# Performance work log

Measured on AMD Instinct MI355X. Metric: run time of the kernel, lower is better.

The kernel has to match this reference:

```python
import jax, jax.numpy as jnp
import numpy as np

HEADS = 8
HEIGHT = 512
WIDTH = 512
LATENT = 64  # height // 8
N_INST = 8


def setup_inputs() -> dict:
    key = jax.random.key(0)
    ks = jax.random.split(key, 8)
    C, Cx, L, N = 320, 768, 77, N_INST
    HW = LATENT * LATENT
    hidden_states = jax.random.normal(ks[0], (2, HW, C), jnp.float32)
    encoder_hidden_states = jax.random.normal(ks[1], (N + 3, L, Cx), jnp.float32)
    # non-degenerate normalized boxes (x0, y0, x1, y1)
    rng = np.random.default_rng(0)
    x0 = rng.uniform(0.0, 0.5, (N,)).astype(np.float32)
    y0 = rng.uniform(0.0, 0.5, (N,)).astype(np.float32)
    x1 = (x0 + rng.uniform(0.2, 0.45, (N,))).astype(np.float32)
    y1 = (y0 + rng.uniform(0.2, 0.45, (N,))).astype(np.float32)
    bboxes = jnp.asarray(np.stack([x0, y0, x1, y1], axis=-1)[None], jnp.float32)  # (1, N, 4)
    s = 0.02
    Wq = jax.random.normal(ks[2], (C, C), jnp.float32) * s
    Wk = jax.random.normal(ks[3], (Cx, C), jnp.float32) * s
    Wv = jax.random.normal(ks[4], (Cx, C), jnp.float32) * s
    Wo = jax.random.normal(ks[5], (C, C), jnp.float32) * s
    bo = jnp.zeros((C,), jnp.float32)
    return dict(hidden_states=hidden_states, encoder_hidden_states=encoder_hidden_states,
                bboxes=bboxes, Wq=Wq, Wk=Wk, Wv=Wv, Wo=Wo, bo=bo)


def _heads(x):
    # (B, S, H*D) -> (B*H, S, D)   [diffusers head_to_batch_dim]
    B, S, C = x.shape
    D = C // HEADS
    return x.reshape(B, S, HEADS, D).transpose(0, 2, 1, 3).reshape(B * HEADS, S, D)


def _unheads(x):
    # (B*H, S, D) -> (B, S, H*D)   [diffusers batch_to_head_dim]
    BH, S, D = x.shape
    B = BH // HEADS
    return x.reshape(B, HEADS, S, D).transpose(0, 2, 1, 3).reshape(B, S, HEADS * D)


def _forward(hidden_states, encoder_hidden_states, bboxes, Wq, Wk, Wv, Wo, bo):
    N = bboxes.shape[1]
    HW = hidden_states.shape[1]
    # drop the extra (MIGC) text embedding row, as in the processor
    ehs = encoder_hidden_states[:-1]  # (N+2, L, Cx)
    # batch = [uncond, cond repeated instance_num+1 times]
    hs = jnp.concatenate([hidden_states[:1],
                          jnp.repeat(hidden_states[1:2], N + 1, axis=0)], axis=0)  # (N+2, HW, C)
    q = _heads(hs @ Wq)
    k = _heads(ehs @ Wk)
    v = _heads(ehs @ Wv)
    scale = 1.0 / jnp.sqrt(jnp.asarray(q.shape[-1], q.dtype))
    probs = jax.nn.softmax(jnp.einsum('bqd,bkd->bqk', q, k) * scale, axis=-1)  # ((N+2)*H, HW, L)
    out = _unheads(jnp.einsum('bqk,bkd->bqd', probs, v))  # (N+2, HW, C)
    out = out @ Wo + bo
    hs_uncond = out[:1]
    cond_ca = out[1:][None]  # (1, N+1, HW, C)
    # rasterize per-instance bbox masks at full res (int() truncation == floor for positives)
    b = bboxes[0]  # (N, 4) = x0, y0, x1, y1
    w_min = jnp.floor(WIDTH * b[:, 0])[:, None, None]
    w_max = jnp.floor(WIDTH * b[:, 2])[:, None, None]
    h_min = jnp.floor(HEIGHT * b[:, 1])[:, None, None]
    h_max = jnp.floor(HEIGHT * b[:, 3])[:, None, None]
    rows = jnp.arange(HEIGHT, dtype=jnp.float32)[None, :, None]
    cols = jnp.arange(WIDTH, dtype=jnp.float32)[None, None, :]
    masks = ((rows >= h_min) & (rows < h_max) & (cols >= w_min) & (cols < w_max)).astype(jnp.float32)  # (N,H,W)
    gmask = jax.image.resize(masks, (N, LATENT, LATENT), method='bilinear')  # (N, 64, 64)
    # NaiveFuser: phase weights = [0.1 (full prompt), 10*mask_i], normalized sum over phases
    phase_w = jnp.concatenate([jnp.full((1, HW), 0.1, jnp.float32),
                               gmask.reshape(N, HW) * 10.0], axis=0)  # (N+1, HW)
    w = phase_w[None, :, :, None]  # (1, N+1, HW, 1)
    fused = (cond_ca * w).sum(axis=1) / (w.sum(axis=1) + 1e-6)  # (1, HW, C)
    return jnp.concatenate([hs_uncond, fused], axis=0)  # (2, HW, C)


def reference(hidden_states, encoder_hidden_states, bboxes, Wq, Wk, Wv, Wo, bo):
    return _forward(hidden_states, encoder_hidden_states, bboxes, Wq, Wk, Wv, Wo, bo)
```

## Files before the change

kernel.cpp:

```cpp
#include <hip/hip_runtime.h>
#include <math.h>

#define HW 4096
#define C 320
#define CX 768
#define L 77
#define NB 10
#define NH 8
#define HD 40
#define NINST 8
#define SCALE 0.15811388300841898f
#define PSTR 104
#define KSTR 48
#define VSTR 104
#define XSTR 328
#define KBH (80 * KSTR)
#define VBH (48 * VSTR)
#define KVCP 264

#define SEG_KV   130
#define MASK_U0  130
#define PAD_U0   146
#define WPK_U0   226
#define NPREP    276

typedef _Float16 half8v __attribute__((ext_vector_type(8)));
typedef _Float16 half4v __attribute__((ext_vector_type(4)));
typedef float f32x4 __attribute__((ext_vector_type(4)));

__device__ __forceinline__ float axis_profile(int o, float lo, float hi) {
    float num = 0.f, den = 0.f;
    int j0 = 8 * o - 4;
#pragma unroll
    for (int t = 0; t < 16; ++t) {
        int j = j0 + t;
        float wt = 1.0f - fabsf((float)t - 7.5f) * 0.125f;
        if (j >= 0 && j < 512) {
            den += wt;
            float fj = (float)j;
            if (fj >= lo && fj < hi) num += wt;
        }
    }
    return num / den;
}

__device__ __forceinline__ half8v cvt8(float4 a, float4 b) {
    half8v h = {(_Float16)a.x, (_Float16)a.y, (_Float16)a.z, (_Float16)a.w,
                (_Float16)b.x, (_Float16)b.y, (_Float16)b.z, (_Float16)b.w};
    return h;
}

__global__ __launch_bounds__(256) void prep_kernel(
        const float* __restrict__ bboxes, const float* __restrict__ ehs,
        const float* __restrict__ Wq, const float* __restrict__ Wk,
        const float* __restrict__ Wv, const float* __restrict__ Wo,
        float* __restrict__ wPh, float* __restrict__ wSum,
        _Float16* __restrict__ WqT, _Float16* __restrict__ WoT,
        _Float16* __restrict__ VTg, _Float16* __restrict__ Khp) {
    __shared__ __align__(16) unsigned char psm[34048];
    int bx = blockIdx.x, tid = threadIdx.x;

    if (bx < SEG_KV) {
        const int K = CX, M = NB * L;
        int lane = tid & 63, wave = tid >> 6;
        int m0 = (bx / 10) * 64 + wave * 16;
        int n0 = (bx % 10) * 64;
        int lr = lane & 15, kq = (lane >> 4) * 8;
        int arow = m0 + lr; if (arow >= M) arow = M - 1;
        const float* ap = ehs + (size_t)arow * K + kq;
        const float* W = (n0 < C) ? Wk : Wv;
        int colbase = (n0 < C) ? n0 : n0 - C;
        _Float16* Bs = (_Float16*)psm;
        f32x4 acc0 = {0.f,0.f,0.f,0.f}, acc1 = acc0, acc2 = acc0, acc3 = acc0;
        for (int c3 = 0; c3 < 3; ++c3) {
            int k0c = c3 * 256;
            __syncthreads();
            for (int i = tid; i < 64 * 256; i += 256) {
                int col = i & 63, k = i >> 6;
                Bs[col * KVCP + k] = (_Float16)W[(size_t)(k0c + k) * C + colbase + col];
            }
            __syncthreads();
#pragma unroll
            for (int k0 = 0; k0 < 256; k0 += 32) {
                float4 a0 = *(const float4*)(ap + k0c + k0);
                float4 a1 = *(const float4*)(ap + k0c + k0 + 4);
                half8v af = cvt8(a0, a1);
                half8v b0 = *(const half8v*)&Bs[(0 * 16 + lr) * KVCP + kq + k0];
                half8v b1 = *(const half8v*)&Bs[(1 * 16 + lr) * KVCP + kq + k0];
                half8v b2 = *(const half8v*)&Bs[(2 * 16 + lr) * KVCP + kq + k0];
                half8v b3 = *(const half8v*)&Bs[(3 * 16 + lr) * KVCP + kq + k0];
                acc0 = __builtin_amdgcn_mfma_f32_16x16x32_f16(af, b0, acc0, 0, 0, 0);
                acc1 = __builtin_amdgcn_mfma_f32_16x16x32_f16(af, b1, acc1, 0, 0, 0);
                acc2 = __builtin_amdgcn_mfma_f32_16x16x32_f16(af, b2, acc2, 0, 0, 0);
                acc3 = __builtin_amdgcn_mfma_f32_16x16x32_f16(af, b3, acc3, 0, 0, 0);
            }
        }
        int rb = m0 + ((lane >> 4) << 2);
        f32x4 accs[4] = {acc0, acc1, acc2, acc3};
#pragma unroll
        for (int t = 0; t < 4; ++t) {
            int col = n0 + t * 16 + lr;
#pragma unroll
            for (int r = 0; r < 4; ++r) {
                int row = rb + r;
                if (row < M) {
                    int bb = row / 77;
                    int key = row - bb * 77;
                    if (col < C) {
                        int h = col / HD, d = col - h * HD;
                        Khp[((size_t)(bb * 8 + h) * 80 + key) * KSTR + d] = (_Float16)accs[t][r];
                    } else {
                        int ch = col - C;
                        int h = ch / HD, d = ch - h * HD;
                        VTg[((size_t)(bb * 8 + h) * 48 + d) * VSTR + key] = (_Float16)accs[t][r];
                    }
                }
            }
        }
    } else if (bx < PAD_U0) {
        float* sw_s = (float*)psm;
        float* sh_s = (float*)psm + 512;
        int oyb = (bx - MASK_U0) * 4;
        for (int i = tid; i < NINST * 64; i += 256) {
            int n = i >> 6, ox = i & 63;
            float lo = floorf(512.f * bboxes[n * 4 + 0]);
            float hi = floorf(512.f * bboxes[n * 4 + 2]);
            sw_s[n * 64 + ox] = axis_profile(ox, lo, hi);
        }
        if (tid < NINST * 4) {
            int n = tid >> 2, oy = tid & 3;
            float lo = floorf(512.f * bboxes[n * 4 + 1]);
            float hi = floorf(512.f * bboxes[n * 4 + 3]);
            sh_s[n * 4 + oy] = axis_profile(oyb + oy, lo, hi);
        }
        __syncthreads();
        int oy = tid >> 6, ox = tid & 63;
        int hw = (oyb + oy) * 64 + ox;
        float sum = 0.1f;
        wPh[hw] = 0.1f;
#pragma unroll
        for (int n = 0; n < NINST; ++n) {
            float wv = 10.f * sh_s[n * 4 + oy] * sw_s[n * 64 + ox];
            wPh[(n + 1) * HW + hw] = wv;
            sum += wv;
        }
        wSum[hw] = sum;
    } else if (bx < WPK_U0) {
        int bh = bx - PAD_U0;
        _Float16* Vb = VTg + (size_t)bh * VBH;
        for (int i = tid; i < 832; i += 256) {
            int dd = i / 104, key = i - dd * 104;
            Vb[(size_t)(40 + dd) * VSTR + key] = (_Float16)((dd == 0 && key < 77) ? 1.f : 0.f);
        }
        for (int i = tid; i < 1080; i += 256) {
            int dd = i / 27, key = 77 + i - dd * 27;
            Vb[(size_t)dd * VSTR + key] = (_Float16)0.f;
        }
        _Float16* Kb = Khp + (size_t)bh * KBH;
        for (int i = tid; i < 144; i += 256) {
            int key = 77 + i / 48, dd = i - (i / 48) * 48;
            Kb[(size_t)key * KSTR + dd] = (_Float16)0.f;
        }
    } else {
        float (*tile)[65] = (float (*)[65])psm;
        int zz = bx - WPK_U0;
        int z = zz / 25, inner = zz - z * 25;
        int by = inner / 5, bx2 = inner - by * 5;
        const float* W = z ? Wo : Wq;
        _Float16* WT = z ? WoT : WqT;
        int kt = by * 64, nt = bx2 * 64;
#pragma unroll
        for (int p = 0; p < 16; ++p) {
            int idx = p * 256 + tid;
            int k = idx >> 6, n = idx & 63;
            tile[k][n] = W[(size_t)(kt + k) * C + nt + n];
        }
        __syncthreads();
#pragma unroll
        for (int p = 0; p < 16; ++p) {
            int idx = p * 256 + tid;
            int n = idx >> 6, k = idx & 63;
            WT[(size_t)(nt + n) * C + kt + k] = (_Float16)tile[k][n];
        }
    }
}

__global__ __launch_bounds__(512, 1) void attn_oproj(
        const float* __restrict__ hs,
        const _Float16* __restrict__ WqT,
        const _Float16* __restrict__ Khp,
        const _Float16* __restrict__ VTg,
        const float* __restrict__ wPh,
        const float* __restrict__ wSum,
        const _Float16* __restrict__ WoT,
        const float* __restrict__ bo,
        float* __restrict__ Out) {
    __shared__ _Float16 smem[NH * 2 * 16 * PSTR + 32 * XSTR];
    _Float16* Xs = smem + NH * 2 * 16 * PSTR;

    const int tid = threadIdx.x;
    const int wave = tid >> 6, lane = tid & 63;
    const int head = wave;
    const int qrow0 = blockIdx.x * 16;
    const int c = lane & 15, quad = lane >> 4;
    _Float16* pl0 = smem + (size_t)(wave * 2) * 16 * PSTR;
    _Float16* pl1 = pl0 + 16 * PSTR;
    half8v zero8 = {(_Float16)0.f,(_Float16)0.f,(_Float16)0.f,(_Float16)0.f,
                    (_Float16)0.f,(_Float16)0.f,(_Float16)0.f,(_Float16)0.f};

#pragma unroll
    for (int i = 0; i < 4; ++i) {
        int idx = i * 64 + lane;
        if (idx < 224) {
            int buf = idx / 112;
            int rem = idx - buf * 112;
            int row = rem / 7, ch = rem - row * 7;
            _Float16* pb = buf ? pl1 : pl0;
            *(half8v*)&pb[row * PSTR + 40 + ch * 8] = zero8;
        }
    }

    {
        const float* bu = hs + (size_t)(qrow0 + c) * C + quad * 8;
        const float* bc = bu + (size_t)HW * C;
        f32x4 qa0[3] = {}, qa1[3] = {};
        for (int k0 = 0; k0 < C; k0 += 32) {
            float4 u0 = *(const float4*)(bu + k0);
            float4 u1 = *(const float4*)(bu + k0 + 4);
            float4 c0 = *(const float4*)(bc + k0);
            float4 c1 = *(const float4*)(bc + k0 + 4);
            half8v hu = cvt8(u0, u1);
            half8v hc = cvt8(c0, c1);
#pragma unroll
            for (int t = 0; t < 3; ++t) {
                const _Float16* ap = WqT + (size_t)(head * HD + t * 16 + c) * C + quad * 8 + k0;
                half8v af = *(const half8v*)ap;
                qa0[t] = __builtin_amdgcn_mfma_f32_16x16x32_f16(af, hu, qa0[t], 0, 0, 0);
                qa1[t] = __builtin_amdgcn_mfma_f32_16x16x32_f16(af, hc, qa1[t], 0, 0, 0);
            }
        }
#pragma unroll
        for (int t = 0; t < 3; ++t) {
            if (t < 2 || quad < 2) {
                half4v h0 = {(_Float16)(qa0[t][0] * SCALE), (_Float16)(qa0[t][1] * SCALE),
                             (_Float16)(qa0[t][2] * SCALE), (_Float16)(qa0[t][3] * SCALE)};
                half4v h1 = {(_Float16)(qa1[t][0] * SCALE), (_Float16)(qa1[t][1] * SCALE),
                             (_Float16)(qa1[t][2] * SCALE), (_Float16)(qa1[t][3] * SCALE)};
                *(half4v*)(pl0 + c * PSTR + t * 16 + quad * 4) = h0;
                *(half4v*)(pl1 + c * PSTR + t * 16 + quad * 4) = h1;
            }
        }
    }
    half8v qu0 = *(const half8v*)(pl0 + (size_t)c * PSTR + quad * 8);
    half8v qu1 = *(const half8v*)(pl0 + (size_t)c * PSTR + 32 + quad * 8);
    half8v qc0 = *(const half8v*)(pl1 + (size_t)c * PSTR + quad * 8);
    half8v qc1 = *(const half8v*)(pl1 + (size_t)c * PSTR + 32 + quad * 8);

    f32x4 oacc[3] = {};
    const int srcl = 32 + c;

    for (int b = 0; b < NB; ++b) {
        const _Float16* Kb = Khp + (size_t)(b * 8 + head) * KBH;
        const _Float16* Vb = VTg + (size_t)(b * 8 + head) * VBH;
        half8v qb0 = b ? qc0 : qu0;
        half8v qb1 = b ? qc1 : qu1;
        float w = b ? wPh[(size_t)(b - 1) * HW + qrow0 + c] : 1.f;

        f32x4 s[5];
#pragma unroll
        for (int u = 0; u < 5; ++u) {
            half8v ka0 = *(const half8v*)&Kb[(u * 16 + c) * KSTR + quad * 8];
            half8v ka1 = *(const half8v*)&Kb[(u * 16 + c) * KSTR + 32 + quad * 8];
            f32x4 a = {0.f,0.f,0.f,0.f};
            a = __builtin_amdgcn_mfma_f32_16x16x32_f16(ka0, qb0, a, 0, 0, 0);
            a = __builtin_amdgcn_mfma_f32_16x16x32_f16(ka1, qb1, a, 0, 0, 0);
            s[u] = a;
        }

#pragma unroll
        for (int u = 0; u < 5; ++u) {
            half4v h = {(_Float16)__expf(s[u][0]), (_Float16)__expf(s[u][1]),
                        (_Float16)__expf(s[u][2]), (_Float16)__expf(s[u][3])};
            *(half4v*)(pl0 + c * PSTR + u * 16 + quad * 4) = h;
        }
        half8v p0 = *(const half8v*)(pl0 + (size_t)c * PSTR + quad * 8);
        half8v p1 = *(const half8v*)(pl0 + (size_t)c * PSTR + 32 + quad * 8);
        half8v p2 = *(const half8v*)(pl0 + (size_t)c * PSTR + 64 + quad * 8);

        f32x4 ox[3];
#pragma unroll
        for (int t = 0; t < 3; ++t) {
            half8v va0 = *(const half8v*)&Vb[(t * 16 + c) * VSTR + quad * 8];
            half8v va1 = *(const half8v*)&Vb[(t * 16 + c) * VSTR + 32 + quad * 8];
            half8v va2 = *(const half8v*)&Vb[(t * 16 + c) * VSTR + 64 + quad * 8];
            f32x4 a = {0.f,0.f,0.f,0.f};
            a = __builtin_amdgcn_mfma_f32_16x16x32_f16(va0, p0, a, 0, 0, 0);
            a = __builtin_amdgcn_mfma_f32_16x16x32_f16(va1, p1, a, 0, 0, 0);
            a = __builtin_amdgcn_mfma_f32_16x16x32_f16(va2, p2, a, 0, 0, 0);
            ox[t] = a;
        }

        float l = __shfl(ox[2][0], srcl, 64);

        if (b == 0) {
            float rin = 1.0f / l;
#pragma unroll
            for (int t = 0; t < 3; ++t) {
                if (t < 2 || quad < 2) {
                    half4v h = {(_Float16)(ox[t][0] * rin), (_Float16)(ox[t][1] * rin),
                                (_Float16)(ox[t][2] * rin), (_Float16)(ox[t][3] * rin)};
                    *(half4v*)(Xs + (size_t)c * XSTR + head * HD + t * 16 + quad * 4) = h;
                }
            }
        } else {
            float rf = w / l;
#pragma unroll
            for (int t = 0; t < 3; ++t) {
                oacc[t][0] += ox[t][0] * rf;
                oacc[t][1] += ox[t][1] * rf;
                oacc[t][2] += ox[t][2] * rf;
                oacc[t][3] += ox[t][3] * rf;
            }
        }
    }

#pragma unroll
    for (int t = 0; t < 3; ++t) {
        if (t < 2 || quad < 2) {
            half4v h = {(_Float16)oacc[t][0], (_Float16)oacc[t][1],
                        (_Float16)oacc[t][2], (_Float16)oacc[t][3]};
            *(half4v*)(Xs + (size_t)(16 + c) * XSTR + head * HD + t * 16 + quad * 4) = h;
        }
    }
    __syncthreads();

    {
        int mt = wave & 1;
        int np = wave >> 1;
        f32x4 acc[5] = {};
#pragma unroll
        for (int k0 = 0; k0 < C; k0 += 32) {
            half8v af = *(const half8v*)&Xs[(size_t)(mt * 16 + c) * XSTR + k0 + quad * 8];
#pragma unroll
            for (int tt = 0; tt < 5; ++tt) {
                const _Float16* bp = WoT + (size_t)(np * 80 + tt * 16 + c) * C + k0 + quad * 8;
                half8v bf = *(const half8v*)bp;
                acc[tt] = __builtin_amdgcn_mfma_f32_16x16x32_f16(af, bf, acc[tt], 0, 0, 0);
            }
        }
#pragma unroll
        for (int tt = 0; tt < 5; ++tt) {
            int col = np * 80 + tt * 16 + c;
            float bv = bo[col];
#pragma unroll
            for (int r = 0; r < 4; ++r) {
                int rr = quad * 4 + r;
                float v = acc[tt][r];
                size_t row;
                if (mt == 0) {
                    v += bv;
                    row = (size_t)qrow0 + rr;
                } else {
                    float ws = wSum[qrow0 + rr];
                    v = (v + bv * ws) / (ws + 1e-6f);
                    row = (size_t)HW + qrow0 + rr;
                }
                Out[row * C + col] = v;
            }
        }
    }
}

extern "C" void kernel_launch(void* const* d_in, const int* in_sizes, int n_in,
                              void* d_out, int out_size, void* d_ws, size_t ws_size,
                              hipStream_t stream) {
    const float* hs   = (const float*)d_in[0];
    const float* ehs  = (const float*)d_in[1];
    const float* bbox = (const float*)d_in[2];
    const float* Wq   = (const float*)d_in[3];
    const float* Wk   = (const float*)d_in[4];
    const float* Wv   = (const float*)d_in[5];
    const float* Wo   = (const float*)d_in[6];
    const float* bo   = (const float*)d_in[7];
    float* out = (float*)d_out;

    float* wPh  = (float*)d_ws;
    float* wSum = wPh + (size_t)9 * HW;
    _Float16* WqT = (_Float16*)(wSum + HW);
    _Float16* WoT = WqT + (size_t)C * C;
    _Float16* Khp = WoT + (size_t)C * C;
    _Float16* VTg = Khp + (size_t)80 * KBH;

    prep_kernel<<<dim3(NPREP), 256, 0, stream>>>(bbox, ehs, Wq, Wk, Wv, Wo,
                                                 wPh, wSum, WqT, WoT, VTg, Khp);
    attn_oproj<<<dim3(HW / 16), 512, 0, stream>>>(hs, WqT, Khp, VTg, wPh, wSum,
                                                  WoT, bo, out);
}
```

Baseline: 147.8 us.

## Software-pipeline K loads across batches and drop LDS staging in KV projection

The attention loop is fully unrolled over the ten batches with double-buffered K fragments, so the next batch's K is fetched while the current batch's scores are computed, and V is loaded at the start of each batch. The P scratch buffer now alternates between two LDS regions. Separately, the KV projection GEMM no longer stages transposed weights in shared memory with barriers; each lane reads strided fp32 weights directly from global memory. This cuts LDS use and synchronisation, but the direct loads are uncoalesced scalar reads, and the unrolled loop raises register pressure.

```diff
diff --git a/kernel.cpp b/kernel.cpp
--- a/kernel.cpp
+++ b/kernel.cpp
@@ -16,7 +16,6 @@
 #define XSTR 328
 #define KBH (80 * KSTR)
 #define VBH (48 * VSTR)
-#define KVCP 264
 
 #define SEG_KV   130
 #define MASK_U0  130
@@ -57,7 +56,7 @@
         float* __restrict__ wPh, float* __restrict__ wSum,
         _Float16* __restrict__ WqT, _Float16* __restrict__ WoT,
         _Float16* __restrict__ VTg, _Float16* __restrict__ Khp) {
-    __shared__ __align__(16) unsigned char psm[34048];
+    __shared__ __align__(16) unsigned char psm[16640];
     int bx = blockIdx.x, tid = threadIdx.x;
 
     if (bx < SEG_KV) {
@@ -68,38 +67,38 @@
         int lr = lane & 15, kq = (lane >> 4) * 8;
         int arow = m0 + lr; if (arow >= M) arow = M - 1;
         const float* ap = ehs + (size_t)arow * K + kq;
-        const float* W = (n0 < C) ? Wk : Wv;
-        int colbase = (n0 < C) ? n0 : n0 - C;
-        _Float16* Bs = (_Float16*)psm;
+        const float* wp[4];
+        int cols[4];
+#pragma unroll
+        for (int t = 0; t < 4; ++t) {
+            int col = n0 + t * 16 + lr;
+            cols[t] = col;
+            wp[t] = (col < C) ? (Wk + col) : (Wv + (col - C));
+        }
         f32x4 acc0 = {0.f,0.f,0.f,0.f}, acc1 = acc0, acc2 = acc0, acc3 = acc0;
-        for (int c3 = 0; c3 < 3; ++c3) {
-            int k0c = c3 * 256;
-            __syncthreads();
-            for (int i = tid; i < 64 * 256; i += 256) {
-                int col = i & 63, k = i >> 6;
-                Bs[col * KVCP + k] = (_Float16)W[(size_t)(k0c + k) * C + colbase + col];
-            }
-            __syncthreads();
-#pragma unroll
-            for (int k0 = 0; k0 < 256; k0 += 32) {
-                float4 a0 = *(const float4*)(ap + k0c + k0);
-                float4 a1 = *(const float4*)(ap + k0c + k0 + 4);
-                half8v af = cvt8(a0, a1);
-                half8v b0 = *(const half8v*)&Bs[(0 * 16 + lr) * KVCP + kq + k0];
-                half8v b1 = *(const half8v*)&Bs[(1 * 16 + lr) * KVCP + kq + k0];
-                half8v b2 = *(const half8v*)&Bs[(2 * 16 + lr) * KVCP + kq + k0];
-                half8v b3 = *(const half8v*)&Bs[(3 * 16 + lr) * KVCP + kq + k0];
-                acc0 = __builtin_amdgcn_mfma_f32_16x16x32_f16(af, b0, acc0, 0, 0, 0);
-                acc1 = __builtin_amdgcn_mfma_f32_16x16x32_f16(af, b1, acc1, 0, 0, 0);
-                acc2 = __builtin_amdgcn_mfma_f32_16x16x32_f16(af, b2, acc2, 0, 0, 0);
-                acc3 = __builtin_amdgcn_mfma_f32_16x16x32_f16(af, b3, acc3, 0, 0, 0);
-            }
+        for (int k0 = 0; k0 < K; k0 += 32) {
+            float4 a0 = *(const float4*)(ap + k0);
+            float4 a1 = *(const float4*)(ap + k0 + 4);
+            half8v af = cvt8(a0, a1);
+            half8v bf0, bf1, bf2, bf3;
+#pragma unroll
+            for (int j = 0; j < 8; ++j) {
+                size_t kk = (size_t)(k0 + kq + j) * C;
+                bf0[j] = (_Float16)wp[0][kk];
+                bf1[j] = (_Float16)wp[1][kk];
+                bf2[j] = (_Float16)wp[2][kk];
+                bf3[j] = (_Float16)wp[3][kk];
+            }
+            acc0 = __builtin_amdgcn_mfma_f32_16x16x32_f16(af, bf0, acc0, 0, 0, 0);
+            acc1 = __builtin_amdgcn_mfma_f32_16x16x32_f16(af, bf1, acc1, 0, 0, 0);
+            acc2 = __builtin_amdgcn_mfma_f32_16x16x32_f16(af, bf2, acc2, 0, 0, 0);
+            acc3 = __builtin_amdgcn_mfma_f32_16x16x32_f16(af, bf3, acc3, 0, 0, 0);
         }
         int rb = m0 + ((lane >> 4) << 2);
         f32x4 accs[4] = {acc0, acc1, acc2, acc3};
 #pragma unroll
         for (int t = 0; t < 4; ++t) {
-            int col = n0 + t * 16 + lr;
+            int col = cols[t];
 #pragma unroll
             for (int r = 0; r < 4; ++r) {
                 int row = rb + r;
@@ -185,6 +184,79 @@
     }
 }
 
+#define LOADK(K0, K1, bidx)                                                    \
+    {                                                                          \
+        const _Float16* Kb_ = Khp + (size_t)((bidx) * 8 + head) * KBH;         \
+        _Pragma("unroll")                                                      \
+        for (int u = 0; u < 5; ++u) {                                          \
+            K0[u] = *(const half8v*)&Kb_[(u * 16 + c) * KSTR + quad * 8];      \
+            K1[u] = *(const half8v*)&Kb_[(u * 16 + c) * KSTR + 32 + quad * 8]; \
+        }                                                                      \
+    }
+
+#define BATCH(b, K0, K1, PB, PREFETCH_STMT)                                        \
+    {                                                                              \
+        const _Float16* Vb_ = VTg + (size_t)((b) * 8 + head) * VBH;                \
+        half8v va0_[3], va1_[3], va2_[3];                                          \
+        _Pragma("unroll")                                                          \
+        for (int t = 0; t < 3; ++t) {                                              \
+            va0_[t] = *(const half8v*)&Vb_[(t * 16 + c) * VSTR + quad * 8];        \
+            va1_[t] = *(const half8v*)&Vb_[(t * 16 + c) * VSTR + 32 + quad * 8];   \
+            va2_[t] = *(const half8v*)&Vb_[(t * 16 + c) * VSTR + 64 + quad * 8];   \
+        }                                                                          \
+        float w_ = (b) ? wPh[(size_t)((b) - 1) * HW + qrow0 + c] : 1.f;            \
+        half8v qb0_ = (b) ? qc0 : qu0;                                             \
+        half8v qb1_ = (b) ? qc1 : qu1;                                             \
+        f32x4 s_[5];                                                               \
+        _Pragma("unroll")                                                          \
+        for (int u = 0; u < 5; ++u) {                                              \
+            f32x4 a_ = {0.f, 0.f, 0.f, 0.f};                                       \
+            a_ = __builtin_amdgcn_mfma_f32_16x16x32_f16(K0[u], qb0_, a_, 0, 0, 0); \
+            a_ = __builtin_amdgcn_mfma_f32_16x16x32_f16(K1[u], qb1_, a_, 0, 0, 0); \
+            s_[u] = a_;                                                            \
+        }                                                                          \
+        PREFETCH_STMT;                                                             \
+        _Pragma("unroll")                                                          \
+        for (int u = 0; u < 5; ++u) {                                              \
+            half4v h_ = {(_Float16)__expf(s_[u][0]), (_Float16)__expf(s_[u][1]),   \
+                         (_Float16)__expf(s_[u][2]), (_Float16)__expf(s_[u][3])};  \
+            *(half4v*)((PB) + c * PSTR + u * 16 + quad * 4) = h_;                  \
+        }                                                                          \
+        half8v p0_ = *(const half8v*)((PB) + (size_t)c * PSTR + quad * 8);         \
+        half8v p1_ = *(const half8v*)((PB) + (size_t)c * PSTR + 32 + quad * 8);    \
+        half8v p2_ = *(const half8v*)((PB) + (size_t)c * PSTR + 64 + quad * 8);    \
+        f32x4 ox_[3];                                                              \
+        _Pragma("unroll")                                                          \
+        for (int t = 0; t < 3; ++t) {                                              \
+            f32x4 a_ = {0.f, 0.f, 0.f, 0.f};                                       \
+            a_ = __builtin_amdgcn_mfma_f32_16x16x32_f16(va0_[t], p0_, a_, 0, 0, 0);\
+            a_ = __builtin_amdgcn_mfma_f32_16x16x32_f16(va1_[t], p1_, a_, 0, 0, 0);\
+            a_ = __builtin_amdgcn_mfma_f32_16x16x32_f16(va2_[t], p2_, a_, 0, 0, 0);\
+            ox_[t] = a_;                                                           \
+        }                                                                          \
+        float l_ = __shfl(ox_[2][0], srcl, 64);                                    \
+        if ((b) == 0) {                                                            \
+            float rin_ = 1.0f / l_;                                                \
+            _Pragma("unroll")                                                      \
+            for (int t = 0; t < 3; ++t) {                                          \
+                if (t < 2 || quad < 2) {                                           \
+                    half4v h_ = {(_Float16)(ox_[t][0] * rin_), (_Float16)(ox_[t][1] * rin_),  \
+                                 (_Float16)(ox_[t][2] * rin_), (_Float16)(ox_[t][3] * rin_)}; \
+                    *(half4v*)(Xs + (size_t)c * XSTR + head * HD + t * 16 + quad * 4) = h_;   \
+                }                                                                  \
+            }                                                                      \
+        } else {                                                                   \
+            float rf_ = w_ / l_;                                                   \
+            _Pragma("unroll")                                                      \
+            for (int t = 0; t < 3; ++t) {                                          \
+                oacc[t][0] += ox_[t][0] * rf_;                                     \
+                oacc[t][1] += ox_[t][1] * rf_;                                     \
+                oacc[t][2] += ox_[t][2] * rf_;                                     \
+                oacc[t][3] += ox_[t][3] * rf_;                                     \
+            }                                                                      \
+        }                                                                          \
+    }
+
 __global__ __launch_bounds__(512, 1) void attn_oproj(
         const float* __restrict__ hs,
         const _Float16* __restrict__ WqT,
@@ -259,70 +331,18 @@
     f32x4 oacc[3] = {};
     const int srcl = 32 + c;
 
-    for (int b = 0; b < NB; ++b) {
-        const _Float16* Kb = Khp + (size_t)(b * 8 + head) * KBH;
-        const _Float16* Vb = VTg + (size_t)(b * 8 + head) * VBH;
-        half8v qb0 = b ? qc0 : qu0;
-        half8v qb1 = b ? qc1 : qu1;
-        float w = b ? wPh[(size_t)(b - 1) * HW + qrow0 + c] : 1.f;
-
-        f32x4 s[5];
-#pragma unroll
-        for (int u = 0; u < 5; ++u) {
-            half8v ka0 = *(const half8v*)&Kb[(u * 16 + c) * KSTR + quad * 8];
-            half8v ka1 = *(const half8v*)&Kb[(u * 16 + c) * KSTR + 32 + quad * 8];
-            f32x4 a = {0.f,0.f,0.f,0.f};
-            a = __builtin_amdgcn_mfma_f32_16x16x32_f16(ka0, qb0, a, 0, 0, 0);
-            a = __builtin_amdgcn_mfma_f32_16x16x32_f16(ka1, qb1, a, 0, 0, 0);
-            s[u] = a;
-        }
-
-#pragma unroll
-        for (int u = 0; u < 5; ++u) {
-            half4v h = {(_Float16)__expf(s[u][0]), (_Float16)__expf(s[u][1]),
-                        (_Float16)__expf(s[u][2]), (_Float16)__expf(s[u][3])};
-            *(half4v*)(pl0 + c * PSTR + u * 16 + quad * 4) = h;
-        }
-        half8v p0 = *(const half8v*)(pl0 + (size_t)c * PSTR + quad * 8);
-        half8v p1 = *(const half8v*)(pl0 + (size_t)c * PSTR + 32 + quad * 8);
-        half8v p2 = *(const half8v*)(pl0 + (size_t)c * PSTR + 64 + quad * 8);
-
-        f32x4 ox[3];
-#pragma unroll
-        for (int t = 0; t < 3; ++t) {
-            half8v va0 = *(const half8v*)&Vb[(t * 16 + c) * VSTR + quad * 8];
-            half8v va1 = *(const half8v*)&Vb[(t * 16 + c) * VSTR + 32 + quad * 8];
-            half8v va2 = *(const half8v*)&Vb[(t * 16 + c) * VSTR + 64 + quad * 8];
-            f32x4 a = {0.f,0.f,0.f,0.f};
-            a = __builtin_amdgcn_mfma_f32_16x16x32_f16(va0, p0, a, 0, 0, 0);
-            a = __builtin_amdgcn_mfma_f32_16x16x32_f16(va1, p1, a, 0, 0, 0);
-            a = __builtin_amdgcn_mfma_f32_16x16x32_f16(va2, p2, a, 0, 0, 0);
-            ox[t] = a;
-        }
-
-        float l = __shfl(ox[2][0], srcl, 64);
-
-        if (b == 0) {
-            float rin = 1.0f / l;
-#pragma unroll
-            for (int t = 0; t < 3; ++t) {
-                if (t < 2 || quad < 2) {
-                    half4v h = {(_Float16)(ox[t][0] * rin), (_Float16)(ox[t][1] * rin),
-                                (_Float16)(ox[t][2] * rin), (_Float16)(ox[t][3] * rin)};
-                    *(half4v*)(Xs + (size_t)c * XSTR + head * HD + t * 16 + quad * 4) = h;
-                }
-            }
-        } else {
-            float rf = w / l;
-#pragma unroll
-            for (int t = 0; t < 3; ++t) {
-                oacc[t][0] += ox[t][0] * rf;
-                oacc[t][1] += ox[t][1] * rf;
-                oacc[t][2] += ox[t][2] * rf;
-                oacc[t][3] += ox[t][3] * rf;
-            }
-        }
-    }
+    half8v kA0[5], kA1[5], kB0[5], kB1[5];
+    LOADK(kA0, kA1, 0);
+    BATCH(0, kA0, kA1, pl0, LOADK(kB0, kB1, 1));
+    BATCH(1, kB0, kB1, pl1, LOADK(kA0, kA1, 2));
+    BATCH(2, kA0, kA1, pl0, LOADK(kB0, kB1, 3));
+    BATCH(3, kB0, kB1, pl1, LOADK(kA0, kA1, 4));
+    BATCH(4, kA0, kA1, pl0, LOADK(kB0, kB1, 5));
+    BATCH(5, kB0, kB1, pl1, LOADK(kA0, kA1, 6));
+    BATCH(6, kA0, kA1, pl0, LOADK(kB0, kB1, 7));
+    BATCH(7, kB0, kB1, pl1, LOADK(kA0, kA1, 8));
+    BATCH(8, kA0, kA1, pl0, LOADK(kB0, kB1, 9));
+    BATCH(9, kB0, kB1, pl1, ((void)0));
 
 #pragma unroll
     for (int t = 0; t < 3; ++t) {
```

After: 146.4 us. Within noise of the previous version (-1.0%).

## Split attention batch loop across two wave groups with 1024-thread blocks

Applied to the files above, without the earlier changes.

Doubles the attention block to 1024 threads so two groups of eight waves each handle half of the ten batch entries (even/odd) for every head. The conditional partial sums from both groups go to separate shared-memory rows and are added in the output projection through an extra MFMA. This shortens each wave's serial loop over batches and adds more waves for latency hiding, at the cost of more shared memory, higher register pressure under launch_bounds(1024), and half the waves sitting idle during the projection. The Q staging for the second group also has to run correctly, and that part of the code is hidden.

```diff
diff --git a/kernel.cpp b/kernel.cpp
--- a/kernel.cpp
+++ b/kernel.cpp
@@ -185,7 +185,7 @@
     }
 }
 
-__global__ __launch_bounds__(512, 1) void attn_oproj(
+__global__ __launch_bounds__(1024) void attn_oproj(
         const float* __restrict__ hs,
         const _Float16* __restrict__ WqT,
         const _Float16* __restrict__ Khp,
@@ -195,12 +195,13 @@
         const _Float16* __restrict__ WoT,
         const float* __restrict__ bo,
         float* __restrict__ Out) {
-    __shared__ _Float16 smem[NH * 2 * 16 * PSTR + 32 * XSTR];
-    _Float16* Xs = smem + NH * 2 * 16 * PSTR;
+    __shared__ _Float16 smem[16 * 2 * 16 * PSTR + 48 * XSTR];
+    _Float16* Xs = smem + 16 * 2 * 16 * PSTR;
 
     const int tid = threadIdx.x;
     const int wave = tid >> 6, lane = tid & 63;
-    const int head = wave;
+    const int head = wave & 7;
+    const int hb = wave >> 3;
     const int qrow0 = blockIdx.x * 16;
     const int c = lane & 15, quad = lane >> 4;
     _Float16* pl0 = smem + (size_t)(wave * 2) * 16 * PSTR;
@@ -259,7 +260,9 @@
     f32x4 oacc[3] = {};
     const int srcl = 32 + c;
 
-    for (int b = 0; b < NB; ++b) {
+#pragma unroll
+    for (int i = 0; i < 5; ++i) {
+        int b = hb + 2 * i;
         const _Float16* Kb = Khp + (size_t)(b * 8 + head) * KBH;
         const _Float16* Vb = VTg + (size_t)(b * 8 + head) * VBH;
         half8v qb0 = b ? qc0 : qu0;
@@ -324,28 +327,39 @@
         }
     }
 
-#pragma unroll
-    for (int t = 0; t < 3; ++t) {
-        if (t < 2 || quad < 2) {
-            half4v h = {(_Float16)oacc[t][0], (_Float16)oacc[t][1],
-                        (_Float16)oacc[t][2], (_Float16)oacc[t][3]};
-            *(half4v*)(Xs + (size_t)(16 + c) * XSTR + head * HD + t * 16 + quad * 4) = h;
+    {
+        int xrow = (hb ? 32 : 16) + c;
+#pragma unroll
+        for (int t = 0; t < 3; ++t) {
+            if (t < 2 || quad < 2) {
+                half4v h = {(_Float16)oacc[t][0], (_Float16)oacc[t][1],
+                            (_Float16)oacc[t][2], (_Float16)oacc[t][3]};
+                *(half4v*)(Xs + (size_t)xrow * XSTR + head * HD + t * 16 + quad * 4) = h;
+            }
         }
     }
     __syncthreads();
 
-    {
+    if (hb == 0) {
         int mt = wave & 1;
         int np = wave >> 1;
         f32x4 acc[5] = {};
 #pragma unroll
         for (int k0 = 0; k0 < C; k0 += 32) {
-            half8v af = *(const half8v*)&Xs[(size_t)(mt * 16 + c) * XSTR + k0 + quad * 8];
+            half8v af0 = zero8, af1 = zero8;
+            if (mt == 0) {
+                af0 = *(const half8v*)&Xs[(size_t)c * XSTR + k0 + quad * 8];
+            } else {
+                af0 = *(const half8v*)&Xs[(size_t)(16 + c) * XSTR + k0 + quad * 8];
+                af1 = *(const half8v*)&Xs[(size_t)(32 + c) * XSTR + k0 + quad * 8];
+            }
 #pragma unroll
             for (int tt = 0; tt < 5; ++tt) {
                 const _Float16* bp = WoT + (size_t)(np * 80 + tt * 16 + c) * C + k0 + quad * 8;
                 half8v bf = *(const half8v*)bp;
-                acc[tt] = __builtin_amdgcn_mfma_f32_16x16x32_f16(af, bf, acc[tt], 0, 0, 0);
+                acc[tt] = __builtin_amdgcn_mfma_f32_16x16x32_f16(af0, bf, acc[tt], 0, 0, 0);
+                if (mt == 1)
+                    acc[tt] = __builtin_amdgcn_mfma_f32_16x16x32_f16(af1, bf, acc[tt], 0, 0, 0);
             }
         }
 #pragma unroll
@@ -393,6 +407,6 @@
 
     prep_kernel<<<dim3(NPREP), 256, 0, stream>>>(bbox, ehs, Wq, Wk, Wv, Wo,
                                                  wPh, wSum, WqT, WoT, VTg, Khp);
-    attn_oproj<<<dim3(HW / 16), 512, 0, stream>>>(hs, WqT, Khp, VTg, wPh, wSum,
-                                                  WoT, bo, out);
+    attn_oproj<<<dim3(HW / 16), 1024, 0, stream>>>(hs, WqT, Khp, VTg, wPh, wSum,
+                                                   WoT, bo, out);
 }
```

Result: slower. 163.2 us (+10.4%).

## Pre-convert hidden states to fp16 in prep and read K/V weights directly

Applied to the files above, without the earlier changes.

Adds a segment of prep blocks that converts both hidden-state batches to fp16 in the workspace, so the attention kernel loads half-precision activations for the Q projection instead of converting fp32 in the inner loop. Separately, the K/V projection blocks stop staging weight tiles in LDS with barriers and instead gather eight strided fp32 weight elements per lane straight from global memory. The hidden-state conversion adds an extra fp32 read and fp16 write round trip plus 2560 more prep blocks. The strided, uncoalesced weight gathers may cost more than the shared-memory staging they replace.

```diff
diff --git a/kernel.cpp b/kernel.cpp
--- a/kernel.cpp
+++ b/kernel.cpp
@@ -16,13 +16,14 @@
 #define XSTR 328
 #define KBH (80 * KSTR)
 #define VBH (48 * VSTR)
-#define KVCP 264
 
 #define SEG_KV   130
 #define MASK_U0  130
 #define PAD_U0   146
 #define WPK_U0   226
-#define NPREP    276
+#define CVT_U0   276
+#define N_CVT1   (2 * HW * C / 4)
+#define NPREP    (CVT_U0 + N_CVT1 / 256)
 
 typedef _Float16 half8v __attribute__((ext_vector_type(8)));
 typedef _Float16 half4v __attribute__((ext_vector_type(4)));
@@ -51,13 +52,15 @@
 }
 
 __global__ __launch_bounds__(256) void prep_kernel(
-        const float* __restrict__ bboxes, const float* __restrict__ ehs,
+        const float* __restrict__ bboxes, const float* __restrict__ hs,
+        const float* __restrict__ ehs,
         const float* __restrict__ Wq, const float* __restrict__ Wk,
         const float* __restrict__ Wv, const float* __restrict__ Wo,
         float* __restrict__ wPh, float* __restrict__ wSum,
+        _Float16* __restrict__ hsH,
         _Float16* __restrict__ WqT, _Float16* __restrict__ WoT,
         _Float16* __restrict__ VTg, _Float16* __restrict__ Khp) {
-    __shared__ __align__(16) unsigned char psm[34048];
+    __shared__ __align__(16) unsigned char psm[16900];
     int bx = blockIdx.x, tid = threadIdx.x;
 
     if (bx < SEG_KV) {
@@ -68,38 +71,38 @@
         int lr = lane & 15, kq = (lane >> 4) * 8;
         int arow = m0 + lr; if (arow >= M) arow = M - 1;
         const float* ap = ehs + (size_t)arow * K + kq;
-        const float* W = (n0 < C) ? Wk : Wv;
-        int colbase = (n0 < C) ? n0 : n0 - C;
-        _Float16* Bs = (_Float16*)psm;
+        const float* wp[4];
+        int cols[4];
+#pragma unroll
+        for (int t = 0; t < 4; ++t) {
+            int col = n0 + t * 16 + lr;
+            cols[t] = col;
+            wp[t] = (col < C) ? (Wk + col) : (Wv + (col - C));
+        }
         f32x4 acc0 = {0.f,0.f,0.f,0.f}, acc1 = acc0, acc2 = acc0, acc3 = acc0;
-        for (int c3 = 0; c3 < 3; ++c3) {
-            int k0c = c3 * 256;
-            __syncthreads();
-            for (int i = tid; i < 64 * 256; i += 256) {
-                int col = i & 63, k = i >> 6;
-                Bs[col * KVCP + k] = (_Float16)W[(size_t)(k0c + k) * C + colbase + col];
-            }
-            __syncthreads();
-#pragma unroll
-            for (int k0 = 0; k0 < 256; k0 += 32) {
-                float4 a0 = *(const float4*)(ap + k0c + k0);
-                float4 a1 = *(const float4*)(ap + k0c + k0 + 4);
-                half8v af = cvt8(a0, a1);
-                half8v b0 = *(const half8v*)&Bs[(0 * 16 + lr) * KVCP + kq + k0];
-                half8v b1 = *(const half8v*)&Bs[(1 * 16 + lr) * KVCP + kq + k0];
-                half8v b2 = *(const half8v*)&Bs[(2 * 16 + lr) * KVCP + kq + k0];
-                half8v b3 = *(const half8v*)&Bs[(3 * 16 + lr) * KVCP + kq + k0];
-                acc0 = __builtin_amdgcn_mfma_f32_16x16x32_f16(af, b0, acc0, 0, 0, 0);
-                acc1 = __builtin_amdgcn_mfma_f32_16x16x32_f16(af, b1, acc1, 0, 0, 0);
-                acc2 = __builtin_amdgcn_mfma_f32_16x16x32_f16(af, b2, acc2, 0, 0, 0);
-                acc3 = __builtin_amdgcn_mfma_f32_16x16x32_f16(af, b3, acc3, 0, 0, 0);
-            }
+        for (int k0 = 0; k0 < K; k0 += 32) {
+            float4 a0 = *(const float4*)(ap + k0);
+            float4 a1 = *(const float4*)(ap + k0 + 4);
+            half8v af = cvt8(a0, a1);
+            half8v bf0, bf1, bf2, bf3;
+#pragma unroll
+            for (int j = 0; j < 8; ++j) {
+                size_t kk = (size_t)(k0 + kq + j) * C;
+                bf0[j] = (_Float16)wp[0][kk];
+                bf1[j] = (_Float16)wp[1][kk];
+                bf2[j] = (_Float16)wp[2][kk];
+                bf3[j] = (_Float16)wp[3][kk];
+            }
+            acc0 = __builtin_amdgcn_mfma_f32_16x16x32_f16(af, bf0, acc0, 0, 0, 0);
+            acc1 = __builtin_amdgcn_mfma_f32_16x16x32_f16(af, bf1, acc1, 0, 0, 0);
+            acc2 = __builtin_amdgcn_mfma_f32_16x16x32_f16(af, bf2, acc2, 0, 0, 0);
+            acc3 = __builtin_amdgcn_mfma_f32_16x16x32_f16(af, bf3, acc3, 0, 0, 0);
         }
         int rb = m0 + ((lane >> 4) << 2);
         f32x4 accs[4] = {acc0, acc1, acc2, acc3};
 #pragma unroll
         for (int t = 0; t < 4; ++t) {
-            int col = n0 + t * 16 + lr;
+            int col = cols[t];
 #pragma unroll
             for (int r = 0; r < 4; ++r) {
                 int row = rb + r;
@@ -161,7 +164,7 @@
             int key = 77 + i / 48, dd = i - (i / 48) * 48;
             Kb[(size_t)key * KSTR + dd] = (_Float16)0.f;
         }
-    } else {
+    } else if (bx < CVT_U0) {
         float (*tile)[65] = (float (*)[65])psm;
         int zz = bx - WPK_U0;
         int z = zz / 25, inner = zz - z * 25;
@@ -182,11 +185,16 @@
             int n = idx >> 6, k = idx & 63;
             WT[(size_t)(nt + n) * C + kt + k] = (_Float16)tile[k][n];
         }
+    } else {
+        int i = (bx - CVT_U0) * 256 + tid;
+        float4 v = ((const float4*)hs)[i];
+        half4v h = {(_Float16)v.x, (_Float16)v.y, (_Float16)v.z, (_Float16)v.w};
+        ((half4v*)hsH)[i] = h;
     }
 }
 
 __global__ __launch_bounds__(512, 1) void attn_oproj(
-        const float* __restrict__ hs,
+        const _Float16* __restrict__ hsH,
         const _Float16* __restrict__ WqT,
         const _Float16* __restrict__ Khp,
         const _Float16* __restrict__ VTg,
@@ -221,16 +229,12 @@
     }
 
     {
-        const float* bu = hs + (size_t)(qrow0 + c) * C + quad * 8;
-        const float* bc = bu + (size_t)HW * C;
+        const _Float16* bu = hsH + (size_t)(qrow0 + c) * C + quad * 8;
+        const _Float16* bc = bu + (size_t)HW * C;
         f32x4 qa0[3] = {}, qa1[3] = {};
         for (int k0 = 0; k0 < C; k0 += 32) {
-            float4 u0 = *(const float4*)(bu + k0);
-            float4 u1 = *(const float4*)(bu + k0 + 4);
-            float4 c0 = *(const float4*)(bc + k0);
-            float4 c1 = *(const float4*)(bc + k0 + 4);
-            half8v hu = cvt8(u0, u1);
-            half8v hc = cvt8(c0, c1);
+            half8v hu = *(const half8v*)(bu + k0);
+            half8v hc = *(const half8v*)(bc + k0);
 #pragma unroll
             for (int t = 0; t < 3; ++t) {
                 const _Float16* ap = WqT + (size_t)(head * HD + t * 16 + c) * C + quad * 8 + k0;
@@ -390,9 +394,10 @@
     _Float16* WoT = WqT + (size_t)C * C;
     _Float16* Khp = WoT + (size_t)C * C;
     _Float16* VTg = Khp + (size_t)80 * KBH;
-
-    prep_kernel<<<dim3(NPREP), 256, 0, stream>>>(bbox, ehs, Wq, Wk, Wv, Wo,
-                                                 wPh, wSum, WqT, WoT, VTg, Khp);
-    attn_oproj<<<dim3(HW / 16), 512, 0, stream>>>(hs, WqT, Khp, VTg, wPh, wSum,
+    _Float16* hsH = VTg + (size_t)80 * VBH;
+
+    prep_kernel<<<dim3(NPREP), 256, 0, stream>>>(bbox, hs, ehs, Wq, Wk, Wv, Wo,
+                                                 wPh, wSum, hsH, WqT, WoT, VTg, Khp);
+    attn_oproj<<<dim3(HW / 16), 512, 0, stream>>>(hsH, WqT, Khp, VTg, wPh, wSum,
                                                   WoT, bo, out);
 }
```

Measured after the change: 144.3 us. -2.4%, faster.
